# Performance work log

Measured on AMD Instinct MI355X. Metric: run time of the kernel, lower is better.

## Reference

```python
import jax, jax.numpy as jnp
import numpy as np

B = 16384
DIM = 1024
HEADS = 16
LN_EPS = 1e-5


def setup_inputs() -> dict:
    key = jax.random.key(0)
    ks = jax.random.split(key, 8)
    d = DIM
    s = 0.02
    return {
        "x_u": jax.random.normal(ks[0], (B, d), dtype=jnp.float32),
        "x_m": jax.random.normal(ks[1], (B, d), dtype=jnp.float32),
        # MHA m2u (path 1): packed in_proj [3d, d] like torch, out_proj [d, d]
        "w_qkv1": (jax.random.normal(ks[2], (3 * d, d), dtype=jnp.float32) * s),
        "b_qkv1": jnp.zeros((3 * d,), dtype=jnp.float32),
        "w_o1": (jax.random.normal(ks[3], (d, d), dtype=jnp.float32) * s),
        "b_o1": jnp.zeros((d,), dtype=jnp.float32),
        # MHA u2m (path 2)
        "w_qkv2": (jax.random.normal(ks[4], (3 * d, d), dtype=jnp.float32) * s),
        "b_qkv2": jnp.zeros((3 * d,), dtype=jnp.float32),
        "w_o2": (jax.random.normal(ks[5], (d, d), dtype=jnp.float32) * s),
        "b_o2": jnp.zeros((d,), dtype=jnp.float32),
        # proj head: LayerNorm(2d) + Linear(2d -> d) + GELU (dropout = eval identity)
        "ln_g": jnp.ones((2 * d,), dtype=jnp.float32),
        "ln_b": jnp.zeros((2 * d,), dtype=jnp.float32),
        "w_proj": (jax.random.normal(ks[6], (d, 2 * d), dtype=jnp.float32) * s),
        "b_proj": jnp.zeros((d,), dtype=jnp.float32),
        "heads": HEADS,
    }


def _mha_single_token(xq, xkv, w_qkv, b_qkv, w_o, b_o, heads):
    # seq_len = 1 cross-attention: softmax over a single key is exactly 1.
    d = xq.shape[-1]
    dh = d // heads
    wq, wk, wv = jnp.split(w_qkv, 3, axis=0)
    bq, bk, bv = jnp.split(b_qkv, 3)
    q = (xq @ wq.T + bq).reshape(-1, heads, dh)   # [B, H, dh]
    k = (xkv @ wk.T + bk).reshape(-1, heads, dh)
    v = (xkv @ wv.T + bv).reshape(-1, heads, dh)
    scores = jnp.sum(q * k, axis=-1) / jnp.sqrt(jnp.asarray(dh, q.dtype))  # [B, H]
    attn = jax.nn.softmax(scores[..., None], axis=-1)  # singleton key axis -> ones
    out = (attn * v).reshape(-1, d)                    # [B, d]
    return out @ w_o.T + b_o


def reference(x_u, x_m, w_qkv1, b_qkv1, w_o1, b_o1,
              w_qkv2, b_qkv2, w_o2, b_o2,
              ln_g, ln_b, w_proj, b_proj, heads):
    # Path 1: Q = x_m, K/V = x_u ; Path 2: Q = x_u, K/V = x_m
    z1 = _mha_single_token(x_m, x_u, w_qkv1, b_qkv1, w_o1, b_o1, heads)
    z2 = _mha_single_token(x_u, x_m, w_qkv2, b_qkv2, w_o2, b_o2, heads)
    z = jnp.concatenate([z1, z2], axis=-1)  # [B, 2d]
    mu = jnp.mean(z, axis=-1, keepdims=True)
    var = jnp.mean(jnp.square(z - mu), axis=-1, keepdims=True)
    zn = (z - mu) * jax.lax.rsqrt(var + LN_EPS) * ln_g + ln_b
    h = zn @ w_proj.T + b_proj               # [B, d]
    return jax.nn.gelu(h, approximate=False)  # torch nn.GELU default = exact erf
```

## Files before the change

### kernel.cpp

```cpp
#include <hip/hip_runtime.h>
#include <cstdint>


#define DIM 1024
#define BROWS 16384

typedef __bf16 bf16x8 __attribute__((ext_vector_type(8)));
typedef float f32x4 __attribute__((ext_vector_type(4)));

__device__ __forceinline__ ushort f2bf(float f) {
    uint32_t u = __builtin_bit_cast(uint32_t, f);
    u = (u + 0x7fffu + ((u >> 16) & 1u)) >> 16;
    return (ushort)u;
}

__device__ __forceinline__ void async_copy16(const void* gsrc, void* ldst) {
    __builtin_amdgcn_global_load_lds(
        (__attribute__((address_space(1))) void*)((uintptr_t)gsrc),
        (__attribute__((address_space(3))) void*)((uint32_t)(uintptr_t)ldst),
        16, 0, 0);
}

__global__ __launch_bounds__(256) void prep_kernel(
        const float* __restrict__ x_u, const float* __restrict__ x_m,
        const float* __restrict__ wqkv1, const float* __restrict__ bqkv1,
        const float* __restrict__ wo1, const float* __restrict__ bo1,
        const float* __restrict__ wqkv2, const float* __restrict__ bqkv2,
        const float* __restrict__ wo2, const float* __restrict__ bo2,
        const float* __restrict__ lng, const float* __restrict__ lnb,
        const float* __restrict__ wproj, const float* __restrict__ bproj,
        ushort* __restrict__ x_bf, ushort* __restrict__ wo12,
        ushort* __restrict__ wvT12, ushort* __restrict__ Wp,
        float* __restrict__ b12, float* __restrict__ Svec, float* __restrict__ Cvec,
        float* __restrict__ sums) {
    const int b = blockIdx.x, t = threadIdx.x;
    __shared__ float red[4][4];
    __shared__ float tls[32][33];

    if (b < 8192) {
        const int n4 = (BROWS * DIM) / 4;
        int i = b * 256 + t;
        const int stride = 8192 * 256;
        const float4* xu4 = (const float4*)x_u;
        const float4* xm4 = (const float4*)x_m;
        ushort4* o4 = (ushort4*)x_bf;
#pragma unroll
        for (int it = 0; it < 4; it++, i += stride) {
            float4 v = (i < n4) ? xu4[i] : xm4[i - n4];
            ushort4 o;
            o.x = f2bf(v.x); o.y = f2bf(v.y); o.z = f2bf(v.z); o.w = f2bf(v.w);
            o4[i] = o;
        }
    } else if (b < 9216) {
        int j = b - 8192;
        float s1 = 0.f, s2 = 0.f, sS = 0.f, sC = 0.f;
        for (int c = t; c < DIM; c += 256) {
            s1 += wo1[j * DIM + c] * bqkv1[2 * DIM + c];
            s2 += wo2[j * DIM + c] * bqkv2[2 * DIM + c];
        }
        for (int c = t; c < 2 * DIM; c += 256) {
            float w = wproj[j * 2 * DIM + c];
            sS += w * lng[c];
            sC += w * lnb[c];
        }
        for (int o = 32; o; o >>= 1) {
            s1 += __shfl_down(s1, o, 64);
            s2 += __shfl_down(s2, o, 64);
            sS += __shfl_down(sS, o, 64);
            sC += __shfl_down(sC, o, 64);
        }
        int wid = t >> 6;
        if ((t & 63) == 0) { red[wid][0] = s1; red[wid][1] = s2; red[wid][2] = sS; red[wid][3] = sC; }
        __syncthreads();
        if (t == 0) {
            s1 = red[0][0] + red[1][0] + red[2][0] + red[3][0];
            s2 = red[0][1] + red[1][1] + red[2][1] + red[3][1];
            sS = red[0][2] + red[1][2] + red[2][2] + red[3][2];
            sC = red[0][3] + red[1][3] + red[2][3] + red[3][3];
            b12[j]       = s1 + bo1[j];
            b12[DIM + j] = s2 + bo2[j];
            Svec[j] = sS;
            Cvec[j] = sC + bproj[j];
        }
    } else if (b < 12288) {
        const int NWO = (DIM * DIM) / 4;
        const int NWP = (DIM * 2 * DIM) / 4;
        const int total = 2 * NWO + NWP;
        int i = (b - 9216) * 256 + t;
        const int stride = 3072 * 256;
        for (; i < total; i += stride) {
            if (i < 2 * NWO) {
                float4 v = (i < NWO) ? ((const float4*)wo1)[i] : ((const float4*)wo2)[i - NWO];
                ushort4 o;
                o.x = f2bf(v.x); o.y = f2bf(v.y); o.z = f2bf(v.z); o.w = f2bf(v.w);
                ((ushort4*)wo12)[i] = o;
            } else {
                int j = i - 2 * NWO;
                float4 v = ((const float4*)wproj)[j];
                int c = (j * 4) & (2 * DIM - 1);
                v.x *= lng[c]; v.y *= lng[c + 1]; v.z *= lng[c + 2]; v.w *= lng[c + 3];
                ushort4 o;
                o.x = f2bf(v.x); o.y = f2bf(v.y); o.z = f2bf(v.z); o.w = f2bf(v.w);
                ((ushort4*)Wp)[j] = o;
            }
        }
    } else if (b < 14336) {
        int tile = b - 12288;
        int z = tile >> 10;
        int t2 = tile & 1023;
        int mt = t2 >> 5, kt = t2 & 31;
        const float* src = z ? wqkv2 : wqkv1;
        int tr = t >> 3;
        int tc4 = (t & 7) * 4;
        const float* p = src + (long)(2 * DIM + mt * 32 + tr) * DIM + kt * 32 + tc4;
        float4 v = *(const float4*)p;
        tls[tr][tc4 + 0] = v.x; tls[tr][tc4 + 1] = v.y;
        tls[tr][tc4 + 2] = v.z; tls[tr][tc4 + 3] = v.w;
        __syncthreads();
        ushort4 o;
        o.x = f2bf(tls[tc4 + 0][tr]);
        o.y = f2bf(tls[tc4 + 1][tr]);
        o.z = f2bf(tls[tc4 + 2][tr]);
        o.w = f2bf(tls[tc4 + 3][tr]);
        *(ushort4*)(wvT12 + (long)z * DIM * DIM + (long)(kt * 32 + tr) * DIM + mt * 32 + tc4) = o;
    } else {
        int i = (b - 14336) * 256 + t;
        ((float4*)sums)[i] = float4{0.f, 0.f, 0.f, 0.f};
    }
}

__global__ __launch_bounds__(256, 2) void gemm_w(
        const ushort* __restrict__ Ag, const ushort* __restrict__ Wg,
        ushort* __restrict__ Cg, int K, int lda, int ldw, int ldc,
        long sAz, long sWz, long sCz) {
    constexpr int BM = 64, BN = 64, BK = 32;
    constexpr int MT = BM / 32;
    constexpr int NT = BN / 32;
    __shared__ __align__(16) ushort As[BM * BK];
    __shared__ __align__(16) ushort Bs[BN * BK];
    const int tid = threadIdx.x;
    const int wid = tid >> 6;
    const int lane = tid & 63;
    const int quad = lane >> 4;
    const int l16 = lane & 15;
    const int waveM = wid >> 1, waveN = wid & 1;
    const int zb = blockIdx.z;

    const ushort* A = Ag + zb * sAz + (long)blockIdx.x * BM * lda;
    const ushort* W = Wg + zb * sWz + (long)blockIdx.y * BN * ldw;

    f32x4 acc[MT][NT] = {};
    constexpr int nA = (BM * BK) / (256 * 8);
    constexpr int nB = (BN * BK) / (256 * 8);
    const int swz = (l16 >> 1) & 3;
    const int rdA = quad ^ swz;
    for (int k0 = 0; k0 < K; k0 += BK) {
#pragma unroll
        for (int c = 0; c < nA; c++) {
            int idx = c * 256 + tid;
            int r = idx >> 2;
            int q = (idx & 3) ^ ((r >> 1) & 3);
            async_copy16(A + (long)r * lda + k0 + q * 8, (char*)As + (c * 256 + wid * 64) * 16);
        }
#pragma unroll
        for (int c = 0; c < nB; c++) {
            int idx = c * 256 + tid;
            int r = idx >> 2;
            int q = (idx & 3) ^ ((r >> 1) & 3);
            async_copy16(W + (long)r * ldw + k0 + q * 8, (char*)Bs + (c * 256 + wid * 64) * 16);
        }
        asm volatile("s_waitcnt vmcnt(0)" ::: "memory");
        __syncthreads();

        bf16x8 af[MT], bfg[NT];
#pragma unroll
        for (int im = 0; im < MT; im++)
            af[im] = *(const bf16x8*)(As + (waveM * (BM / 2) + im * 16 + l16) * BK + rdA * 8);
#pragma unroll
        for (int in = 0; in < NT; in++)
            bfg[in] = *(const bf16x8*)(Bs + (waveN * (BN / 2) + in * 16 + l16) * BK + rdA * 8);
#pragma unroll
        for (int im = 0; im < MT; im++)
#pragma unroll
            for (int in = 0; in < NT; in++)
                acc[im][in] = __builtin_amdgcn_mfma_f32_16x16x32_bf16(
                    af[im], bfg[in], acc[im][in], 0, 0, 0);
        __syncthreads();
    }

    const int gRow0 = blockIdx.x * BM + waveM * (BM / 2) + quad * 4;
    const int gCol0 = blockIdx.y * BN + waveN * (BN / 2) + l16;
    ushort* C = Cg + zb * sCz;
#pragma unroll
    for (int im = 0; im < MT; im++)
#pragma unroll
        for (int in = 0; in < NT; in++) {
            int col = gCol0 + in * 16;
#pragma unroll
            for (int r = 0; r < 4; r++) {
                int row = gRow0 + im * 16 + r;
                C[(long)row * ldc + col] = f2bf(acc[im][in][r]);
            }
        }
}

template <int MODE>
__global__ __launch_bounds__(512, 2) void gemm256(
        const ushort* __restrict__ Ag, const ushort* __restrict__ Wg,
        void* __restrict__ Cg, int K, int lda, int ldw, int ldc,
        long sAz, long sWz, long sCz,
        const float* __restrict__ bias,
        const float* __restrict__ Svec, const float* __restrict__ Cvec,
        float* __restrict__ sumbuf, float* __restrict__ sqbuf) {
    __shared__ __align__(16) ushort As[4 * 8192];
    __shared__ __align__(16) ushort Bs[4 * 8192];
    const int tid = threadIdx.x;
    const int wid = tid >> 6;
    const int lane = tid & 63;
    const int quad = lane >> 4;
    const int l16 = lane & 15;
    const int waveM = wid >> 2;
    const int waveN = wid & 3;
    const int zb = blockIdx.z;
    const int rd = quad ^ ((l16 >> 1) & 3);

    const ushort* A = Ag + zb * sAz + (long)blockIdx.x * 256 * lda;
    const ushort* W = Wg + zb * sWz + (long)blockIdx.y * 256 * ldw;
    const int NTK = K >> 5;

    f32x4 acc[8][4] = {};

#pragma unroll
    for (int u = 0; u < 3; ++u) {
        const int k0 = u << 5;
        char* sa = (char*)As + u * 16384;
        char* sb = (char*)Bs + u * 16384;
#pragma unroll
        for (int rnd = 0; rnd < 2; ++rnd) {
            int idx = rnd * 512 + tid;
            int r = idx >> 2;
            int q = (idx & 3) ^ ((r >> 1) & 3);
            async_copy16(A + (long)r * lda + k0 + q * 8, sa + (rnd * 512 + wid * 64) * 16);
        }
#pragma unroll
        for (int rnd = 0; rnd < 2; ++rnd) {
            int idx = rnd * 512 + tid;
            int r = idx >> 2;
            int q = (idx & 3) ^ ((r >> 1) & 3);
            async_copy16(W + (long)r * ldw + k0 + q * 8, sb + (rnd * 512 + wid * 64) * 16);
        }
    }
    asm volatile("s_waitcnt vmcnt(8)" ::: "memory");
    __builtin_amdgcn_s_barrier();
    asm volatile("" ::: "memory");

    for (int t = 0; t < NTK; ++t) {
        const ushort* as = As + (t & 3) * 8192;
        const ushort* bs = Bs + (t & 3) * 8192;
        const int u = t + 3;
        const bool doStage = (u < NTK);
        char* sa = (char*)As + (u & 3) * 16384;
        char* sb = (char*)Bs + (u & 3) * 16384;
        const int k0u = u << 5;

        bf16x8 af[4], bfg[4];
#pragma unroll
        for (int j = 0; j < 4; ++j)
            bfg[j] = *(const bf16x8*)(bs + (waveN * 64 + j * 16 + l16) * 32 + rd * 8);
#pragma unroll
        for (int i = 0; i < 4; ++i)
            af[i] = *(const bf16x8*)(as + (waveM * 128 + i * 16 + l16) * 32 + rd * 8);
        if (doStage) {
#pragma unroll
            for (int rnd = 0; rnd < 2; ++rnd) {
                int idx = rnd * 512 + tid;
                int r = idx >> 2;
                int q = (idx & 3) ^ ((r >> 1) & 3);
                async_copy16(A + (long)r * lda + k0u + q * 8, sa + (rnd * 512 + wid * 64) * 16);
            }
        }
        __builtin_amdgcn_s_setprio(1);
#pragma unroll
        for (int i = 0; i < 4; ++i)
#pragma unroll
            for (int j = 0; j < 4; ++j)
                acc[i][j] = __builtin_amdgcn_mfma_f32_16x16x32_bf16(
                    af[i], bfg[j], acc[i][j], 0, 0, 0);
        __builtin_amdgcn_s_setprio(0);

#pragma unroll
        for (int i = 0; i < 4; ++i)
            af[i] = *(const bf16x8*)(as + (waveM * 128 + 64 + i * 16 + l16) * 32 + rd * 8);
        if (doStage) {
#pragma unroll
            for (int rnd = 0; rnd < 2; ++rnd) {
                int idx = rnd * 512 + tid;
                int r = idx >> 2;
                int q = (idx & 3) ^ ((r >> 1) & 3);
                async_copy16(W + (long)r * ldw + k0u + q * 8, sb + (rnd * 512 + wid * 64) * 16);
            }
        }
        __builtin_amdgcn_s_setprio(1);
#pragma unroll
        for (int i = 0; i < 4; ++i)
#pragma unroll
            for (int j = 0; j < 4; ++j)
                acc[4 + i][j] = __builtin_amdgcn_mfma_f32_16x16x32_bf16(
                    af[i], bfg[j], acc[4 + i][j], 0, 0, 0);
        __builtin_amdgcn_s_setprio(0);

        if (t < NTK - 1) {
            const int rem = NTK - 1 - t;
            if (rem >= 3)      asm volatile("s_waitcnt vmcnt(8)" ::: "memory");
            else if (rem == 2) asm volatile("s_waitcnt vmcnt(4)" ::: "memory");
            else               asm volatile("s_waitcnt vmcnt(0)" ::: "memory");
            __builtin_amdgcn_s_barrier();
            asm volatile("" ::: "memory");
        }
    }

    const int gRow0 = blockIdx.x * 256 + waveM * 128 + quad * 4;
    const int gCol0 = blockIdx.y * 256 + waveN * 64 + l16;
    if constexpr (MODE == 1) {
        ushort* C = (ushort*)Cg + zb * sCz;
#pragma unroll
        for (int im = 0; im < 8; ++im) {
            float sr[4] = {0.f, 0.f, 0.f, 0.f};
            float qr[4] = {0.f, 0.f, 0.f, 0.f};
#pragma unroll
            for (int in = 0; in < 4; ++in) {
                int col = gCol0 + in * 16;
                float badd = bias[zb * DIM + col];
#pragma unroll
                for (int r = 0; r < 4; ++r) {
                    int row = gRow0 + im * 16 + r;
                    float val = acc[im][in][r] + badd;
                    C[(long)row * ldc + col] = f2bf(val);
                    sr[r] += val;
                    qr[r] += val * val;
                }
            }
#pragma unroll
            for (int r = 0; r < 4; ++r) {
                float s = sr[r], q = qr[r];
#pragma unroll
                for (int o = 1; o < 16; o <<= 1) {
                    s += __shfl_xor(s, o, 64);
                    q += __shfl_xor(q, o, 64);
                }
                if (l16 == 0) {
                    int row = gRow0 + im * 16 + r;
                    atomicAdd(&sumbuf[row], s);
                    atomicAdd(&sqbuf[row], q);
                }
            }
        }
    } else {
        float* O = (float*)Cg;
#pragma unroll
        for (int im = 0; im < 8; ++im) {
#pragma unroll
            for (int r = 0; r < 4; ++r) {
                int row = gRow0 + im * 16 + r;
                float sv = sumbuf[row], qv = sqbuf[row];
                float m = sv * (1.f / 2048.f);
                float var = qv * (1.f / 2048.f) - m * m;
                float rstd = rsqrtf(var + 1e-5f);
#pragma unroll
                for (int in = 0; in < 4; ++in) {
                    int col = gCol0 + in * 16;
                    float h = rstd * (acc[im][in][r] - m * Svec[col]) + Cvec[col];
                    O[(long)row * ldc + col] = 0.5f * h * (1.0f + erff(h * 0.7071067811865475f));
                }
            }
        }
    }
}


extern "C" void kernel_launch(void* const* d_in, const int* in_sizes, int n_in,
                              void* d_out, int out_size, void* d_ws, size_t ws_size,
                              hipStream_t stream) {
    (void)in_sizes; (void)n_in; (void)out_size; (void)ws_size;
    const float* x_u   = (const float*)d_in[0];
    const float* x_m   = (const float*)d_in[1];
    const float* wqkv1 = (const float*)d_in[2];
    const float* bqkv1 = (const float*)d_in[3];
    const float* wo1   = (const float*)d_in[4];
    const float* bo1   = (const float*)d_in[5];
    const float* wqkv2 = (const float*)d_in[6];
    const float* bqkv2 = (const float*)d_in[7];
    const float* wo2   = (const float*)d_in[8];
    const float* bo2   = (const float*)d_in[9];
    const float* lng   = (const float*)d_in[10];
    const float* lnb   = (const float*)d_in[11];
    const float* wproj = (const float*)d_in[12];
    const float* bproj = (const float*)d_in[13];

    char* ws = (char*)d_ws;
    ushort* x_bf  = (ushort*)(ws + 0);
    ushort* wo12  = (ushort*)(ws + 67108864);
    ushort* wvT12 = (ushort*)(ws + 71303168);
    ushort* W12   = (ushort*)(ws + 75497472);
    ushort* Wp    = (ushort*)(ws + 79691776);
    ushort* zbuf  = (ushort*)(ws + 83886080);
    float*  b12   = (float*)(ws + 150994944);
    float*  Svec  = (float*)(ws + 151003136);
    float*  Cvec  = (float*)(ws + 151007232);
    float*  sumbuf= (float*)(ws + 151011328);
    float*  sqbuf = (float*)(ws + 151076864);

    prep_kernel<<<14368, 256, 0, stream>>>(
        x_u, x_m, wqkv1, bqkv1, wo1, bo1, wqkv2, bqkv2, wo2, bo2,
        lng, lnb, wproj, bproj,
        x_bf, wo12, wvT12, Wp, b12, Svec, Cvec, sumbuf);

    gemm_w<<<dim3(16, 16, 2), 256, 0, stream>>>(
        wo12, wvT12, W12, DIM, DIM, DIM, DIM,
        (long)DIM * DIM, (long)DIM * DIM, (long)DIM * DIM);

    gemm256<1><<<dim3(64, 4, 2), 512, 0, stream>>>(
        x_bf, W12, zbuf, DIM, DIM, DIM, 2 * DIM,
        (long)BROWS * DIM, (long)DIM * DIM, (long)DIM,
        b12, nullptr, nullptr, sumbuf, sqbuf);

    gemm256<2><<<dim3(64, 4, 1), 512, 0, stream>>>(
        zbuf, Wp, d_out, 2 * DIM, 2 * DIM, 2 * DIM, DIM,
        0, 0, 0,
        nullptr, Svec, Cvec, sumbuf, sqbuf);
}
```

Measured before the change: 397.0 us.

## Switch main GEMMs to 256x128 tiles with 4 waves and 3-stage pipeline

Replaces the 512-thread 256x256 GEMM with a 256-thread 256x128 tile kernel. Each of the 4 waves now computes a 128x64 sub-tile in a single MFMA burst over 8 A fragments. The LDS pipeline drops from 4 stages to 3, which cuts shared memory so more blocks can be resident. The grid doubles in N, giving more blocks for better CU fill. The cost is less B reuse per loaded A tile and more A traffic from global memory.

```diff
diff --git a/kernel.cpp b/kernel.cpp
--- a/kernel.cpp
+++ b/kernel.cpp
@@ -205,122 +205,110 @@
 }
 
 template <int MODE>
-__global__ __launch_bounds__(512, 2) void gemm256(
+__global__ __launch_bounds__(256, 2) void gemm_bt2(
         const ushort* __restrict__ Ag, const ushort* __restrict__ Wg,
         void* __restrict__ Cg, int K, int lda, int ldw, int ldc,
         long sAz, long sWz, long sCz,
         const float* __restrict__ bias,
         const float* __restrict__ Svec, const float* __restrict__ Cvec,
         float* __restrict__ sumbuf, float* __restrict__ sqbuf) {
-    __shared__ __align__(16) ushort As[4 * 8192];
-    __shared__ __align__(16) ushort Bs[4 * 8192];
+    __shared__ __align__(16) ushort As[3 * 8192];
+    __shared__ __align__(16) ushort Bs[3 * 4096];
     const int tid = threadIdx.x;
     const int wid = tid >> 6;
     const int lane = tid & 63;
     const int quad = lane >> 4;
     const int l16 = lane & 15;
-    const int waveM = wid >> 2;
-    const int waveN = wid & 3;
+    const int waveM = wid >> 1;
+    const int waveN = wid & 1;
     const int zb = blockIdx.z;
     const int rd = quad ^ ((l16 >> 1) & 3);
 
     const ushort* A = Ag + zb * sAz + (long)blockIdx.x * 256 * lda;
-    const ushort* W = Wg + zb * sWz + (long)blockIdx.y * 256 * ldw;
+    const ushort* W = Wg + zb * sWz + (long)blockIdx.y * 128 * ldw;
     const int NTK = K >> 5;
 
     f32x4 acc[8][4] = {};
 
 #pragma unroll
-    for (int u = 0; u < 3; ++u) {
+    for (int u = 0; u < 2; ++u) {
         const int k0 = u << 5;
         char* sa = (char*)As + u * 16384;
-        char* sb = (char*)Bs + u * 16384;
-#pragma unroll
-        for (int rnd = 0; rnd < 2; ++rnd) {
-            int idx = rnd * 512 + tid;
+        char* sb = (char*)Bs + u * 8192;
+#pragma unroll
+        for (int rnd = 0; rnd < 4; ++rnd) {
+            int idx = rnd * 256 + tid;
             int r = idx >> 2;
             int q = (idx & 3) ^ ((r >> 1) & 3);
-            async_copy16(A + (long)r * lda + k0 + q * 8, sa + (rnd * 512 + wid * 64) * 16);
+            async_copy16(A + (long)r * lda + k0 + q * 8, sa + (rnd * 256 + wid * 64) * 16);
         }
 #pragma unroll
         for (int rnd = 0; rnd < 2; ++rnd) {
-            int idx = rnd * 512 + tid;
+            int idx = rnd * 256 + tid;
             int r = idx >> 2;
             int q = (idx & 3) ^ ((r >> 1) & 3);
-            async_copy16(W + (long)r * ldw + k0 + q * 8, sb + (rnd * 512 + wid * 64) * 16);
+            async_copy16(W + (long)r * ldw + k0 + q * 8, sb + (rnd * 256 + wid * 64) * 16);
         }
     }
-    asm volatile("s_waitcnt vmcnt(8)" ::: "memory");
+    asm volatile("s_waitcnt vmcnt(6)" ::: "memory");
     __builtin_amdgcn_s_barrier();
     asm volatile("" ::: "memory");
 
+    int cs = 0, ss = 2;
     for (int t = 0; t < NTK; ++t) {
-        const ushort* as = As + (t & 3) * 8192;
-        const ushort* bs = Bs + (t & 3) * 8192;
-        const int u = t + 3;
-        const bool doStage = (u < NTK);
-        char* sa = (char*)As + (u & 3) * 16384;
-        char* sb = (char*)Bs + (u & 3) * 16384;
-        const int k0u = u << 5;
-
-        bf16x8 af[4], bfg[4];
+        const ushort* as = As + cs * 8192;
+        const ushort* bs = Bs + cs * 4096;
+
+        bf16x8 af[8], bfg[4];
 #pragma unroll
         for (int j = 0; j < 4; ++j)
             bfg[j] = *(const bf16x8*)(bs + (waveN * 64 + j * 16 + l16) * 32 + rd * 8);
 #pragma unroll
-        for (int i = 0; i < 4; ++i)
+        for (int i = 0; i < 8; ++i)
             af[i] = *(const bf16x8*)(as + (waveM * 128 + i * 16 + l16) * 32 + rd * 8);
-        if (doStage) {
-#pragma unroll
-            for (int rnd = 0; rnd < 2; ++rnd) {
-                int idx = rnd * 512 + tid;
+
+        const int u = t + 2;
+        if (u < NTK) {
+            const int k0u = u << 5;
+            char* sa = (char*)As + ss * 16384;
+            char* sb = (char*)Bs + ss * 8192;
+#pragma unroll
+            for (int rnd = 0; rnd < 4; ++rnd) {
+                int idx = rnd * 256 + tid;
                 int r = idx >> 2;
                 int q = (idx & 3) ^ ((r >> 1) & 3);
-                async_copy16(A + (long)r * lda + k0u + q * 8, sa + (rnd * 512 + wid * 64) * 16);
-            }
-        }
+                async_copy16(A + (long)r * lda + k0u + q * 8, sa + (rnd * 256 + wid * 64) * 16);
+            }
+#pragma unroll
+            for (int rnd = 0; rnd < 2; ++rnd) {
+                int idx = rnd * 256 + tid;
+                int r = idx >> 2;
+                int q = (idx & 3) ^ ((r >> 1) & 3);
+                async_copy16(W + (long)r * ldw + k0u + q * 8, sb + (rnd * 256 + wid * 64) * 16);
+            }
+        }
+
         __builtin_amdgcn_s_setprio(1);
 #pragma unroll
-        for (int i = 0; i < 4; ++i)
+        for (int i = 0; i < 8; ++i)
 #pragma unroll
             for (int j = 0; j < 4; ++j)
                 acc[i][j] = __builtin_amdgcn_mfma_f32_16x16x32_bf16(
                     af[i], bfg[j], acc[i][j], 0, 0, 0);
         __builtin_amdgcn_s_setprio(0);
 
-#pragma unroll
-        for (int i = 0; i < 4; ++i)
-            af[i] = *(const bf16x8*)(as + (waveM * 128 + 64 + i * 16 + l16) * 32 + rd * 8);
-        if (doStage) {
-#pragma unroll
-            for (int rnd = 0; rnd < 2; ++rnd) {
-                int idx = rnd * 512 + tid;
-                int r = idx >> 2;
-                int q = (idx & 3) ^ ((r >> 1) & 3);
-                async_copy16(W + (long)r * ldw + k0u + q * 8, sb + (rnd * 512 + wid * 64) * 16);
-            }
-        }
-        __builtin_amdgcn_s_setprio(1);
-#pragma unroll
-        for (int i = 0; i < 4; ++i)
-#pragma unroll
-            for (int j = 0; j < 4; ++j)
-                acc[4 + i][j] = __builtin_amdgcn_mfma_f32_16x16x32_bf16(
-                    af[i], bfg[j], acc[4 + i][j], 0, 0, 0);
-        __builtin_amdgcn_s_setprio(0);
-
         if (t < NTK - 1) {
-            const int rem = NTK - 1 - t;
-            if (rem >= 3)      asm volatile("s_waitcnt vmcnt(8)" ::: "memory");
-            else if (rem == 2) asm volatile("s_waitcnt vmcnt(4)" ::: "memory");
-            else               asm volatile("s_waitcnt vmcnt(0)" ::: "memory");
+            if (t < NTK - 2) asm volatile("s_waitcnt vmcnt(6)" ::: "memory");
+            else             asm volatile("s_waitcnt vmcnt(0)" ::: "memory");
             __builtin_amdgcn_s_barrier();
             asm volatile("" ::: "memory");
         }
+        cs = (cs == 2) ? 0 : cs + 1;
+        ss = (ss == 2) ? 0 : ss + 1;
     }
 
     const int gRow0 = blockIdx.x * 256 + waveM * 128 + quad * 4;
-    const int gCol0 = blockIdx.y * 256 + waveN * 64 + l16;
+    const int gCol0 = blockIdx.y * 128 + waveN * 64 + l16;
     if constexpr (MODE == 1) {
         ushort* C = (ushort*)Cg + zb * sCz;
 #pragma unroll
@@ -419,12 +407,12 @@
         wo12, wvT12, W12, DIM, DIM, DIM, DIM,
         (long)DIM * DIM, (long)DIM * DIM, (long)DIM * DIM);
 
-    gemm256<1><<<dim3(64, 4, 2), 512, 0, stream>>>(
+    gemm_bt2<1><<<dim3(64, 8, 2), 256, 0, stream>>>(
         x_bf, W12, zbuf, DIM, DIM, DIM, 2 * DIM,
         (long)BROWS * DIM, (long)DIM * DIM, (long)DIM,
         b12, nullptr, nullptr, sumbuf, sqbuf);
 
-    gemm256<2><<<dim3(64, 4, 1), 512, 0, stream>>>(
+    gemm_bt2<2><<<dim3(64, 8, 1), 256, 0, stream>>>(
         zbuf, Wp, d_out, 2 * DIM, 2 * DIM, 2 * DIM, DIM,
         0, 0, 0,
         nullptr, Svec, Cvec, sumbuf, sqbuf);
```

Result: no change. 402.9 us (+1.5%).
